# Optimization experiments

Hardware: AMD Instinct MI355X
Metric: run time of the kernel (lower is better)

Reference implementation:

```python
import jax, jax.numpy as jnp
import numpy as np

IDIM = 1024
ODIM = 1024
NHEADS = 16
B, S = 4, 1024


def setup_inputs() -> dict:
    key = jax.random.key(0)
    k1, k2, k3, k4, k5, k6 = jax.random.split(key, 6)
    m_feats = jax.random.normal(k1, (B, S, IDIM), dtype=jnp.float32)
    mask = jax.random.randint(k2, (B, S), 0, 2, dtype=jnp.int32)
    # torch Linear weights stored pre-transposed: y = x @ W + b
    W_c = jax.random.normal(k3, (IDIM, 2 * ODIM), dtype=jnp.float32) * 0.02
    b_c = jnp.zeros((2 * ODIM,), dtype=jnp.float32)
    W_v = jax.random.normal(k4, (IDIM, ODIM), dtype=jnp.float32) * 0.02
    b_v = jnp.zeros((ODIM,), dtype=jnp.float32)
    return {"m_feats": m_feats, "mask": mask, "W_c": W_c, "b_c": b_c, "W_v": W_v, "b_v": b_v}


def reference(m_feats, mask, W_c, b_c, W_v, b_v):
    # dp = 0.0 -> dropout is identity (eval-mode equivalence)
    Bn, Sn, _ = m_feats.shape
    odim = W_v.shape[1]
    dh = odim // NHEADS
    m_k = m_feats @ W_v + b_v            # v_lin  -> keys   [B,S,odim]
    m_trans = m_feats @ W_c + b_c        # c_lin  -> [B,S,2*odim]
    m_q = m_trans[..., :odim]            # queries
    m_v = m_trans[..., odim:]            # values
    mk = m_k.reshape(Bn, Sn, NHEADS, dh)
    mq = m_q.reshape(Bn, Sn, NHEADS, dh)
    mv = m_v.reshape(Bn, Sn, NHEADS, dh)
    # original: scores = K @ Q^T / sqrt(dh); softmax over the Q (last) axis
    scores = jnp.einsum('bihd,bjhd->bhij', mk, mq) / jnp.sqrt(jnp.float32(dh))
    maskf = mask.astype(jnp.float32)
    scores = jnp.where(maskf[:, None, None, :] == 0.0, jnp.float32(-1e9), scores)
    w = jax.nn.softmax(scores, axis=-1)               # [B,H,S,S]
    r = jnp.einsum('bhij,bjhd->bihd', w, mv).reshape(Bn, Sn, odim)
    updated_m = m_feats + r
    return updated_m, w
```

## Files before the change

kernel.cpp:

```cpp
#include <hip/hip_runtime.h>
#include <cstddef>

typedef short short8 __attribute__((ext_vector_type(8)));
typedef float f32x4 __attribute__((ext_vector_type(4)));

#define SS 1024
#define NH 16
#define DH 64
#define NB 4

static __device__ __forceinline__ unsigned short f2bf(float f) {
    union { float f; unsigned int i; } x; x.f = f;
    unsigned int r = x.i + 0x7FFFu + ((x.i >> 16) & 1u);
    return (unsigned short)(r >> 16);
}
static __device__ __forceinline__ float bf2f(unsigned short u) {
    union { unsigned int i; float f; } x; x.i = ((unsigned int)u) << 16;
    return x.f;
}

static __device__ __forceinline__ void g2l16(const void* g, void* l) {
    __builtin_amdgcn_global_load_lds(
        (const __attribute__((address_space(1))) unsigned int*)g,
        (__attribute__((address_space(3))) unsigned int*)l, 16, 0, 0);
}

__global__ __launch_bounds__(256) void prep(const float* __restrict__ mf,
                                            unsigned short* __restrict__ mfb,
                                            const float* __restrict__ Wv,
                                            const float* __restrict__ Wc,
                                            unsigned short* __restrict__ WT) {
    __shared__ float tile[32][33];
    int bx = blockIdx.x;
    int t = threadIdx.x;
    if (bx < 2048) {
        size_t i = ((size_t)bx * 256 + t) * 8;
        float4 v0 = *(const float4*)(mf + i);
        float4 v1 = *(const float4*)(mf + i + 4);
        short8 o;
        o[0] = (short)f2bf(v0.x); o[1] = (short)f2bf(v0.y);
        o[2] = (short)f2bf(v0.z); o[3] = (short)f2bf(v0.w);
        o[4] = (short)f2bf(v1.x); o[5] = (short)f2bf(v1.y);
        o[6] = (short)f2bf(v1.z); o[7] = (short)f2bf(v1.w);
        *(short8*)(mfb + i) = o;
        return;
    }
    bx -= 2048;
    int n0 = (bx % 96) * 32, k0 = (bx / 96) * 32;
    int kr = t >> 3, nc = (t & 7) * 4;
    const float* src; int ld; int nn = n0 + nc;
    if (n0 < 1024) { src = Wv; ld = 1024; } else { src = Wc; ld = 2048; nn -= 1024; }
    float4 v = *(const float4*)(src + (size_t)(k0 + kr) * ld + nn);
    tile[kr][nc + 0] = v.x; tile[kr][nc + 1] = v.y;
    tile[kr][nc + 2] = v.z; tile[kr][nc + 3] = v.w;
    __syncthreads();
    int nr = t >> 3, kc = (t & 7) * 4;
    short4 o;
    o.x = (short)f2bf(tile[kc + 0][nr]); o.y = (short)f2bf(tile[kc + 1][nr]);
    o.z = (short)f2bf(tile[kc + 2][nr]); o.w = (short)f2bf(tile[kc + 3][nr]);
    *(short4*)(WT + (size_t)(n0 + nr) * 1024 + k0 + kc) = o;
}

__global__ __launch_bounds__(256) void gemm_kqv(const unsigned short* __restrict__ A,
                                                const unsigned short* __restrict__ BT,
                                                const float* __restrict__ bv,
                                                const float* __restrict__ bc,
                                                unsigned short* __restrict__ kq,
                                                unsigned short* __restrict__ mvT) {
    __shared__ __align__(16) unsigned short As[2][128 * 32];
    __shared__ __align__(16) unsigned short Bs[2][128 * 32];
    int lin = blockIdx.y * 24 + blockIdx.x;
    int xcd = lin & 7, idx = lin >> 3;
    int cx = xcd & 1, cy = xcd >> 1;
    int xi = idx % 12, yi = idx / 12;
    int n0 = (cx * 12 + xi) * 128;
    int m0 = (cy * 8 + yi) * 128;

    int tid = threadIdx.x, lane = tid & 63, wv = tid >> 6;
    int wm = wv >> 1, wn = wv & 1;
    int lq = lane & 15, quad = lane >> 4;

    f32x4 zero = {0.f, 0.f, 0.f, 0.f};
    f32x4 acc[4][4];
#pragma unroll
    for (int i = 0; i < 4; ++i)
#pragma unroll
        for (int j = 0; j < 4; ++j) acc[i][j] = zero;

    int r0 = tid >> 2, s0 = tid & 3;
    int c0 = s0 ^ ((r0 >> 1) & 3);
    int r1 = (tid + 256) >> 2, s1 = tid & 3;
    int c1 = s1 ^ ((r1 >> 1) & 3);

    const unsigned short* Abase0 = A + (size_t)(m0 + r0) * 1024 + c0 * 8;
    const unsigned short* Abase1 = A + (size_t)(m0 + r1) * 1024 + c1 * 8;
    const unsigned short* Bbase0 = BT + (size_t)(n0 + r0) * 1024 + c0 * 8;
    const unsigned short* Bbase1 = BT + (size_t)(n0 + r1) * 1024 + c1 * 8;

    g2l16(Abase0, As[0] + tid * 8);
    g2l16(Abase1, As[0] + (tid + 256) * 8);
    g2l16(Bbase0, Bs[0] + tid * 8);
    g2l16(Bbase1, Bs[0] + (tid + 256) * 8);
    __syncthreads();

#pragma unroll 2
    for (int t32 = 0; t32 < 32; ++t32) {
        int cur = t32 & 1;
        if (t32 < 31) {
            int nkt = (t32 + 1) * 32;
            g2l16(Abase0 + nkt, As[cur ^ 1] + tid * 8);
            g2l16(Abase1 + nkt, As[cur ^ 1] + (tid + 256) * 8);
            g2l16(Bbase0 + nkt, Bs[cur ^ 1] + tid * 8);
            g2l16(Bbase1 + nkt, Bs[cur ^ 1] + (tid + 256) * 8);
        }

        short8 af[4], bfr[4];
#pragma unroll
        for (int i = 0; i < 4; ++i) {
            int Ra = wm * 64 + i * 16 + lq;
            af[i] = *(const short8*)(As[cur] + Ra * 32 + (quad ^ ((Ra >> 1) & 3)) * 8);
            int Rb = wn * 64 + i * 16 + lq;
            bfr[i] = *(const short8*)(Bs[cur] + Rb * 32 + (quad ^ ((Rb >> 1) & 3)) * 8);
        }
#pragma unroll
        for (int mi = 0; mi < 4; ++mi)
#pragma unroll
            for (int ni = 0; ni < 4; ++ni)
                acc[mi][ni] = __builtin_amdgcn_mfma_f32_16x16x32_bf16(af[mi], bfr[ni], acc[mi][ni], 0, 0, 0);

        __syncthreads();
    }

#pragma unroll
    for (int mi = 0; mi < 4; ++mi) {
#pragma unroll
        for (int ni = 0; ni < 4; ++ni) {
            int colg = n0 + wn * 64 + ni * 16 + lq;
            float bias = (colg < 1024) ? bv[colg] : bc[colg - 1024];
            if (colg < 2048) {
#pragma unroll
                for (int r = 0; r < 4; ++r) {
                    int rowg = m0 + wm * 64 + mi * 16 + quad * 4 + r;
                    kq[(size_t)rowg * 2048 + colg] = f2bf(acc[mi][ni][r] + bias);
                }
            } else {
                int c = colg - 2048;
                int hh = c >> 6, dd = c & 63;
#pragma unroll
                for (int r = 0; r < 4; ++r) {
                    int rowg = m0 + wm * 64 + mi * 16 + quad * 4 + r;
                    int bb = rowg >> 10, jj = rowg & 1023;
                    mvT[((size_t)(bb * NH + hh) * DH + dd) * 1024 + jj] =
                        f2bf(acc[mi][ni][r] + bias);
                }
            }
        }
    }
}

__global__ __launch_bounds__(256, 2) void attn_kernel(const unsigned short* __restrict__ kq,
                                                      const unsigned short* __restrict__ mvT,
                                                      const int* __restrict__ mask,
                                                      const float* __restrict__ m_feats,
                                                      float* __restrict__ out0,
                                                      float* __restrict__ out1) {
    __shared__ __align__(16) unsigned short mk_s[32 * 72];
    __shared__ __align__(16) unsigned short s_exp[32 * 1032];
    __shared__ float wsum[4][32];
    __shared__ float inv_s[32];

    int tid = threadIdx.x;
    int lane = tid & 63, wv = tid >> 6;
    int lq = lane & 15, quad = lane >> 4;

    int blk = ((int)blockIdx.x & 7) * 256 + ((int)blockIdx.x >> 3);
    int it = blk & 31;
    int bh = blk >> 5;
    int h = bh & (NH - 1), b = bh >> 4;
    int i0 = it * 32;

    const float SC = 0.18033688011112042f;
    const unsigned short* mqb = kq + (size_t)b * SS * 2048 + 1024 + h * 64 + quad * 8;
    const int* maskb = mask + (size_t)b * SS;

    short8 qb[2][4][2];
    int qm[2][4];
    float sums[2][4] = {{0.f, 0.f, 0.f, 0.f}, {0.f, 0.f, 0.f, 0.f}};

#define QLOAD(p, s)                                                          \
    {                                                                        \
        int jb_ = (s) * 256 + wv * 64;                                       \
        _Pragma("unroll") for (int js = 0; js < 4; ++js) {                   \
            int jg_ = jb_ + js * 16 + lq;                                    \
            size_t ro_ = (size_t)jg_ * 2048;                                 \
            qb[p][js][0] = *(const short8*)(mqb + ro_);                      \
            qb[p][js][1] = *(const short8*)(mqb + ro_ + 32);                 \
            qm[p][js] = maskb[jg_];                                          \
        }                                                                    \
    }

#define QCOMP(p, s)                                                          \
    {                                                                        \
        int jb_ = (s) * 256 + wv * 64;                                       \
        _Pragma("unroll") for (int js = 0; js < 4; ++js) {                   \
            int jc_ = jb_ + js * 16 + lq;                                    \
            _Pragma("unroll") for (int ti = 0; ti < 2; ++ti) {               \
                f32x4 acc = {0.f, 0.f, 0.f, 0.f};                            \
                acc = __builtin_amdgcn_mfma_f32_16x16x32_bf16(a[ti][0], qb[p][js][0], acc, 0, 0, 0); \
                acc = __builtin_amdgcn_mfma_f32_16x16x32_bf16(a[ti][1], qb[p][js][1], acc, 0, 0, 0); \
                _Pragma("unroll") for (int r = 0; r < 4; ++r) {              \
                    float e = qm[p][js] ? __builtin_amdgcn_exp2f(acc[r] * SC) : 0.f; \
                    sums[ti][r] += e;                                        \
                    s_exp[(ti * 16 + quad * 4 + r) * 1032 + jc_] = f2bf(e);  \
                }                                                            \
            }                                                                \
        }                                                                    \
    }

    QLOAD(0, 0);

    float mf8[2][4];
#pragma unroll
    for (int ti = 0; ti < 2; ++ti)
#pragma unroll
        for (int r = 0; r < 4; ++r) {
            size_t o = (size_t)(b * SS + i0 + ti * 16 + quad * 4 + r) * 1024 + h * 64 + wv * 16 + lq;
            mf8[ti][r] = m_feats[o];
        }

    {
        int row = tid >> 3, ch = tid & 7;
        int4 v = *(const int4*)(kq + (size_t)(b * SS + i0 + row) * 2048 + h * 64 + ch * 8);
        *(int4*)(mk_s + row * 72 + ch * 8) = v;
    }
    QLOAD(1, 1);
    __syncthreads();

    short8 a[2][2];
#pragma unroll
    for (int ti = 0; ti < 2; ++ti) {
        a[ti][0] = *(const short8*)(mk_s + (ti * 16 + lq) * 72 + 0 * 32 + quad * 8);
        a[ti][1] = *(const short8*)(mk_s + (ti * 16 + lq) * 72 + 1 * 32 + quad * 8);
    }

    QCOMP(0, 0); QLOAD(0, 2);
    QCOMP(1, 1); QLOAD(1, 3);
    QCOMP(0, 2);
    QCOMP(1, 3);
#undef QLOAD
#undef QCOMP

    f32x4 racc[2] = {{0.f, 0.f, 0.f, 0.f}, {0.f, 0.f, 0.f, 0.f}};
    const unsigned short* mvb = mvT + ((size_t)bh * DH + wv * 16 + lq) * 1024 + quad * 8;
    size_t wbase = ((size_t)bh * SS + i0) * SS;
    short8 vbuf[4][4];

#define VLOAD(p, ko)                                                         \
    {                                                                        \
        _Pragma("unroll") for (int k2 = 0; k2 < 4; ++k2)                     \
            vbuf[p][k2] = *(const short8*)(mvb + ((ko) * 4 + k2) * 32);      \
    }

#define VCOMP(p, ko)                                                         \
    {                                                                        \
        _Pragma("unroll") for (int k2 = 0; k2 < 4; ++k2) {                   \
            _Pragma("unroll") for (int ti = 0; ti < 2; ++ti) {               \
                short8 ae = *(const short8*)(s_exp + (ti * 16 + lq) * 1032 + ((ko) * 4 + k2) * 32 + quad * 8); \
                racc[ti] = __builtin_amdgcn_mfma_f32_16x16x32_bf16(ae, vbuf[p][k2], racc[ti], 0, 0, 0); \
            }                                                                \
        }                                                                    \
    }

#define WOUT(r)                                                              \
    {                                                                        \
        float iv = inv_s[r];                                                 \
        short4 ev = *(const short4*)(s_exp + (r) * 1032 + tid * 4);          \
        f32x4 wo;                                                            \
        wo[0] = bf2f((unsigned short)ev.x) * iv;                             \
        wo[1] = bf2f((unsigned short)ev.y) * iv;                             \
        wo[2] = bf2f((unsigned short)ev.z) * iv;                             \
        wo[3] = bf2f((unsigned short)ev.w) * iv;                             \
        __builtin_nontemporal_store(wo, (f32x4*)(out1 + wbase + (size_t)(r) * SS + tid * 4)); \
    }

    VLOAD(0, 0); VLOAD(1, 1);

#pragma unroll
    for (int ti = 0; ti < 2; ++ti)
#pragma unroll
        for (int r = 0; r < 4; ++r) {
            float s = sums[ti][r];
            s += __shfl_xor(s, 1); s += __shfl_xor(s, 2);
            s += __shfl_xor(s, 4); s += __shfl_xor(s, 8);
            if (lq == 0) wsum[wv][ti * 16 + quad * 4 + r] = s;
        }
    __syncthreads();
    if (tid < 32) {
        float s = wsum[0][tid] + wsum[1][tid] + wsum[2][tid] + wsum[3][tid];
        inv_s[tid] = 1.0f / s;
    }
    VLOAD(2, 2); VLOAD(3, 3);
    __syncthreads();

    VCOMP(0, 0); VLOAD(0, 4); WOUT(0);  WOUT(1);  WOUT(2);  WOUT(3);
    VCOMP(1, 1); VLOAD(1, 5); WOUT(4);  WOUT(5);  WOUT(6);  WOUT(7);
    VCOMP(2, 2); VLOAD(2, 6); WOUT(8);  WOUT(9);  WOUT(10); WOUT(11);
    VCOMP(3, 3); VLOAD(3, 7); WOUT(12); WOUT(13); WOUT(14); WOUT(15);
    VCOMP(0, 4); WOUT(16); WOUT(17); WOUT(18); WOUT(19);
    VCOMP(1, 5); WOUT(20); WOUT(21); WOUT(22); WOUT(23);
    VCOMP(2, 6); WOUT(24); WOUT(25); WOUT(26); WOUT(27);
    VCOMP(3, 7); WOUT(28); WOUT(29); WOUT(30); WOUT(31);
#undef VLOAD
#undef VCOMP
#undef WOUT

#pragma unroll
    for (int ti = 0; ti < 2; ++ti)
#pragma unroll
        for (int r = 0; r < 4; ++r) {
            int row = ti * 16 + quad * 4 + r;
            size_t o = (size_t)(b * SS + i0 + row) * 1024 + h * 64 + wv * 16 + lq;
            __builtin_nontemporal_store(mf8[ti][r] + racc[ti][r] * inv_s[row], out0 + o);
        }
}

extern "C" void kernel_launch(void* const* d_in, const int* in_sizes, int n_in,
                              void* d_out, int out_size, void* d_ws, size_t ws_size,
                              hipStream_t stream) {
    const float* m_feats = (const float*)d_in[0];
    const int*   mask    = (const int*)d_in[1];
    const float* W_c     = (const float*)d_in[2];
    const float* b_c     = (const float*)d_in[3];
    const float* W_v     = (const float*)d_in[4];
    const float* b_v     = (const float*)d_in[5];

    float* out0 = (float*)d_out;
    float* out1 = out0 + (size_t)NB * SS * 1024;

    unsigned short* mf_bf = (unsigned short*)d_ws;
    unsigned short* WT    = mf_bf + (size_t)4096 * 1024;
    unsigned short* kq    = WT + (size_t)3072 * 1024;
    unsigned short* mvT   = kq + (size_t)4096 * 2048;

    prep<<<dim3(5120), dim3(256), 0, stream>>>(m_feats, mf_bf, W_v, W_c, WT);
    gemm_kqv<<<dim3(24, 32), dim3(256), 0, stream>>>(mf_bf, WT, b_v, b_c, kq, mvT);
    attn_kernel<<<dim3(2048), dim3(256), 0, stream>>>(kq, mvT, mask, m_feats, out0, out1);
}
```

Measured before the change: 375.4 us.

## Double attention row tile to 64 rows with 512-thread blocks

Each attention block now covers 64 query rows using 8 waves instead of 32 rows with 4 waves. Every loaded Q tile is reused across twice as many score rows, which halves the global reads of the Q and V operands per output. The cost is a larger LDS footprint (about 132KB of s_exp), one block per CU, more registers per thread, and a shallower load pipeline in the score phase.

```diff
diff --git a/kernel.cpp b/kernel.cpp
--- a/kernel.cpp
+++ b/kernel.cpp
@@ -158,26 +158,26 @@
     }
 }
 
-__global__ __launch_bounds__(256, 2) void attn_kernel(const unsigned short* __restrict__ kq,
+__global__ __launch_bounds__(512, 1) void attn_kernel(const unsigned short* __restrict__ kq,
                                                       const unsigned short* __restrict__ mvT,
                                                       const int* __restrict__ mask,
                                                       const float* __restrict__ m_feats,
                                                       float* __restrict__ out0,
                                                       float* __restrict__ out1) {
-    __shared__ __align__(16) unsigned short mk_s[32 * 72];
-    __shared__ __align__(16) unsigned short s_exp[32 * 1032];
-    __shared__ float wsum[4][32];
-    __shared__ float inv_s[32];
+    __shared__ __align__(16) unsigned short mk_s[64 * 72];
+    __shared__ __align__(16) unsigned short s_exp[64 * 1032];
+    __shared__ float wsum[8][64];
+    __shared__ float inv_s[64];
 
     int tid = threadIdx.x;
     int lane = tid & 63, wv = tid >> 6;
     int lq = lane & 15, quad = lane >> 4;
 
-    int blk = ((int)blockIdx.x & 7) * 256 + ((int)blockIdx.x >> 3);
-    int it = blk & 31;
-    int bh = blk >> 5;
+    int blk = ((int)blockIdx.x & 7) * 128 + ((int)blockIdx.x >> 3);
+    int it = blk & 15;
+    int bh = blk >> 4;
     int h = bh & (NH - 1), b = bh >> 4;
-    int i0 = it * 32;
+    int i0 = it * 64;
 
     const float SC = 0.18033688011112042f;
     const unsigned short* mqb = kq + (size_t)b * SS * 2048 + 1024 + h * 64 + quad * 8;
@@ -185,11 +185,11 @@
 
     short8 qb[2][4][2];
     int qm[2][4];
-    float sums[2][4] = {{0.f, 0.f, 0.f, 0.f}, {0.f, 0.f, 0.f, 0.f}};
+    float sums[4][4] = {{0.f,0.f,0.f,0.f},{0.f,0.f,0.f,0.f},{0.f,0.f,0.f,0.f},{0.f,0.f,0.f,0.f}};
 
 #define QLOAD(p, s)                                                          \
     {                                                                        \
-        int jb_ = (s) * 256 + wv * 64;                                       \
+        int jb_ = (s) * 512 + wv * 64;                                       \
         _Pragma("unroll") for (int js = 0; js < 4; ++js) {                   \
             int jg_ = jb_ + js * 16 + lq;                                    \
             size_t ro_ = (size_t)jg_ * 2048;                                 \
@@ -201,10 +201,10 @@
 
 #define QCOMP(p, s)                                                          \
     {                                                                        \
-        int jb_ = (s) * 256 + wv * 64;                                       \
+        int jb_ = (s) * 512 + wv * 64;                                       \
         _Pragma("unroll") for (int js = 0; js < 4; ++js) {                   \
             int jc_ = jb_ + js * 16 + lq;                                    \
-            _Pragma("unroll") for (int ti = 0; ti < 2; ++ti) {               \
+            _Pragma("unroll") for (int ti = 0; ti < 4; ++ti) {               \
                 f32x4 acc = {0.f, 0.f, 0.f, 0.f};                            \
                 acc = __builtin_amdgcn_mfma_f32_16x16x32_bf16(a[ti][0], qb[p][js][0], acc, 0, 0, 0); \
                 acc = __builtin_amdgcn_mfma_f32_16x16x32_bf16(a[ti][1], qb[p][js][1], acc, 0, 0, 0); \
@@ -219,13 +219,15 @@
 
     QLOAD(0, 0);
 
+    int wq = wv & 3, tp = wv >> 2;
     float mf8[2][4];
 #pragma unroll
-    for (int ti = 0; ti < 2; ++ti)
+    for (int tt = 0; tt < 2; ++tt)
 #pragma unroll
         for (int r = 0; r < 4; ++r) {
-            size_t o = (size_t)(b * SS + i0 + ti * 16 + quad * 4 + r) * 1024 + h * 64 + wv * 16 + lq;
-            mf8[ti][r] = m_feats[o];
+            size_t o = (size_t)(b * SS + i0 + (tp * 2 + tt) * 16 + quad * 4 + r) * 1024
+                       + h * 64 + wq * 16 + lq;
+            mf8[tt][r] = m_feats[o];
         }
 
     {
@@ -236,22 +238,20 @@
     QLOAD(1, 1);
     __syncthreads();
 
-    short8 a[2][2];
-#pragma unroll
-    for (int ti = 0; ti < 2; ++ti) {
+    short8 a[4][2];
+#pragma unroll
+    for (int ti = 0; ti < 4; ++ti) {
         a[ti][0] = *(const short8*)(mk_s + (ti * 16 + lq) * 72 + 0 * 32 + quad * 8);
         a[ti][1] = *(const short8*)(mk_s + (ti * 16 + lq) * 72 + 1 * 32 + quad * 8);
     }
 
-    QCOMP(0, 0); QLOAD(0, 2);
-    QCOMP(1, 1); QLOAD(1, 3);
-    QCOMP(0, 2);
-    QCOMP(1, 3);
+    QCOMP(0, 0);
+    QCOMP(1, 1);
 #undef QLOAD
 #undef QCOMP
 
     f32x4 racc[2] = {{0.f, 0.f, 0.f, 0.f}, {0.f, 0.f, 0.f, 0.f}};
-    const unsigned short* mvb = mvT + ((size_t)bh * DH + wv * 16 + lq) * 1024 + quad * 8;
+    const unsigned short* mvb = mvT + ((size_t)bh * DH + wq * 16 + lq) * 1024 + quad * 8;
     size_t wbase = ((size_t)bh * SS + i0) * SS;
     short8 vbuf[4][4];
 
@@ -264,29 +264,30 @@
 #define VCOMP(p, ko)                                                         \
     {                                                                        \
         _Pragma("unroll") for (int k2 = 0; k2 < 4; ++k2) {                   \
-            _Pragma("unroll") for (int ti = 0; ti < 2; ++ti) {               \
-                short8 ae = *(const short8*)(s_exp + (ti * 16 + lq) * 1032 + ((ko) * 4 + k2) * 32 + quad * 8); \
-                racc[ti] = __builtin_amdgcn_mfma_f32_16x16x32_bf16(ae, vbuf[p][k2], racc[ti], 0, 0, 0); \
+            _Pragma("unroll") for (int tt = 0; tt < 2; ++tt) {               \
+                short8 ae = *(const short8*)(s_exp + ((tp * 2 + tt) * 16 + lq) * 1032 + ((ko) * 4 + k2) * 32 + quad * 8); \
+                racc[tt] = __builtin_amdgcn_mfma_f32_16x16x32_bf16(ae, vbuf[p][k2], racc[tt], 0, 0, 0); \
             }                                                                \
         }                                                                    \
     }
 
-#define WOUT(r)                                                              \
-    {                                                                        \
-        float iv = inv_s[r];                                                 \
-        short4 ev = *(const short4*)(s_exp + (r) * 1032 + tid * 4);          \
+#define WOUT(pr)                                                             \
+    {                                                                        \
+        int row_ = (pr) * 2 + (tid >> 8);                                    \
+        float iv = inv_s[row_];                                              \
+        short4 ev = *(const short4*)(s_exp + row_ * 1032 + (tid & 255) * 4); \
         f32x4 wo;                                                            \
         wo[0] = bf2f((unsigned short)ev.x) * iv;                             \
         wo[1] = bf2f((unsigned short)ev.y) * iv;                             \
         wo[2] = bf2f((unsigned short)ev.z) * iv;                             \
         wo[3] = bf2f((unsigned short)ev.w) * iv;                             \
-        __builtin_nontemporal_store(wo, (f32x4*)(out1 + wbase + (size_t)(r) * SS + tid * 4)); \
+        __builtin_nontemporal_store(wo, (f32x4*)(out1 + wbase + (size_t)row_ * SS + (tid & 255) * 4)); \
     }
 
     VLOAD(0, 0); VLOAD(1, 1);
 
 #pragma unroll
-    for (int ti = 0; ti < 2; ++ti)
+    for (int ti = 0; ti < 4; ++ti)
 #pragma unroll
         for (int r = 0; r < 4; ++r) {
             float s = sums[ti][r];
@@ -295,8 +296,9 @@
             if (lq == 0) wsum[wv][ti * 16 + quad * 4 + r] = s;
         }
     __syncthreads();
-    if (tid < 32) {
-        float s = wsum[0][tid] + wsum[1][tid] + wsum[2][tid] + wsum[3][tid];
+    if (tid < 64) {
+        float s = wsum[0][tid] + wsum[1][tid] + wsum[2][tid] + wsum[3][tid]
+                + wsum[4][tid] + wsum[5][tid] + wsum[6][tid] + wsum[7][tid];
         inv_s[tid] = 1.0f / s;
     }
     VLOAD(2, 2); VLOAD(3, 3);
@@ -315,12 +317,12 @@
 #undef WOUT
 
 #pragma unroll
-    for (int ti = 0; ti < 2; ++ti)
+    for (int tt = 0; tt < 2; ++tt)
 #pragma unroll
         for (int r = 0; r < 4; ++r) {
-            int row = ti * 16 + quad * 4 + r;
-            size_t o = (size_t)(b * SS + i0 + row) * 1024 + h * 64 + wv * 16 + lq;
-            __builtin_nontemporal_store(mf8[ti][r] + racc[ti][r] * inv_s[row], out0 + o);
+            int row = (tp * 2 + tt) * 16 + quad * 4 + r;
+            size_t o = (size_t)(b * SS + i0 + row) * 1024 + h * 64 + wq * 16 + lq;
+            __builtin_nontemporal_store(mf8[tt][r] + racc[tt][r] * inv_s[row], out0 + o);
         }
 }
 
@@ -344,5 +346,5 @@
 
     prep<<<dim3(5120), dim3(256), 0, stream>>>(m_feats, mf_bf, W_v, W_c, WT);
     gemm_kqv<<<dim3(24, 32), dim3(256), 0, stream>>>(mf_bf, WT, b_v, b_c, kq, mvT);
-    attn_kernel<<<dim3(2048), dim3(256), 0, stream>>>(kq, mvT, mask, m_feats, out0, out1);
-}
+    attn_kernel<<<dim3(1024), dim3(512), 0, stream>>>(kq, mvT, mask, m_feats, out0, out1);
+}
```

Result: slower. 399.4 us (+6.4%).

## Split score computation into two row halves to overlap weight stores with compute

Applied to the files above, without the earlier changes.

The QK^T/exp phase now runs per 16-row half. After the first half, its row sums are reduced and its normalized softmax rows are streamed to the attention-weight output while the second half's scores are computed. This starts the large weight-matrix writes earlier instead of holding them all until the PV phase. In exchange, Q tiles are loaded twice, there is an extra reduction with barriers, and register pressure rises.

```diff
diff --git a/kernel.cpp b/kernel.cpp
--- a/kernel.cpp
+++ b/kernel.cpp
@@ -166,7 +166,7 @@
                                                       float* __restrict__ out1) {
     __shared__ __align__(16) unsigned short mk_s[32 * 72];
     __shared__ __align__(16) unsigned short s_exp[32 * 1032];
-    __shared__ float wsum[4][32];
+    __shared__ float wsum[4][16];
     __shared__ float inv_s[32];
 
     int tid = threadIdx.x;
@@ -199,20 +199,18 @@
         }                                                                    \
     }
 
-#define QCOMP(p, s)                                                          \
+#define QCOMPH(p, s, TI)                                                     \
     {                                                                        \
         int jb_ = (s) * 256 + wv * 64;                                       \
         _Pragma("unroll") for (int js = 0; js < 4; ++js) {                   \
             int jc_ = jb_ + js * 16 + lq;                                    \
-            _Pragma("unroll") for (int ti = 0; ti < 2; ++ti) {               \
-                f32x4 acc = {0.f, 0.f, 0.f, 0.f};                            \
-                acc = __builtin_amdgcn_mfma_f32_16x16x32_bf16(a[ti][0], qb[p][js][0], acc, 0, 0, 0); \
-                acc = __builtin_amdgcn_mfma_f32_16x16x32_bf16(a[ti][1], qb[p][js][1], acc, 0, 0, 0); \
-                _Pragma("unroll") for (int r = 0; r < 4; ++r) {              \
-                    float e = qm[p][js] ? __builtin_amdgcn_exp2f(acc[r] * SC) : 0.f; \
-                    sums[ti][r] += e;                                        \
-                    s_exp[(ti * 16 + quad * 4 + r) * 1032 + jc_] = f2bf(e);  \
-                }                                                            \
+            f32x4 acc = {0.f, 0.f, 0.f, 0.f};                                \
+            acc = __builtin_amdgcn_mfma_f32_16x16x32_bf16(a[TI][0], qb[p][js][0], acc, 0, 0, 0); \
+            acc = __builtin_amdgcn_mfma_f32_16x16x32_bf16(a[TI][1], qb[p][js][1], acc, 0, 0, 0); \
+            _Pragma("unroll") for (int r = 0; r < 4; ++r) {                  \
+                float e = qm[p][js] ? __builtin_amdgcn_exp2f(acc[r] * SC) : 0.f; \
+                sums[TI][r] += e;                                            \
+                s_exp[((TI) * 16 + quad * 4 + r) * 1032 + jc_] = f2bf(e);    \
             }                                                                \
         }                                                                    \
     }
@@ -243,33 +241,24 @@
         a[ti][1] = *(const short8*)(mk_s + (ti * 16 + lq) * 72 + 1 * 32 + quad * 8);
     }
 
-    QCOMP(0, 0); QLOAD(0, 2);
-    QCOMP(1, 1); QLOAD(1, 3);
-    QCOMP(0, 2);
-    QCOMP(1, 3);
-#undef QLOAD
-#undef QCOMP
-
-    f32x4 racc[2] = {{0.f, 0.f, 0.f, 0.f}, {0.f, 0.f, 0.f, 0.f}};
-    const unsigned short* mvb = mvT + ((size_t)bh * DH + wv * 16 + lq) * 1024 + quad * 8;
-    size_t wbase = ((size_t)bh * SS + i0) * SS;
-    short8 vbuf[4][4];
-
-#define VLOAD(p, ko)                                                         \
-    {                                                                        \
-        _Pragma("unroll") for (int k2 = 0; k2 < 4; ++k2)                     \
-            vbuf[p][k2] = *(const short8*)(mvb + ((ko) * 4 + k2) * 32);      \
-    }
-
-#define VCOMP(p, ko)                                                         \
-    {                                                                        \
-        _Pragma("unroll") for (int k2 = 0; k2 < 4; ++k2) {                   \
-            _Pragma("unroll") for (int ti = 0; ti < 2; ++ti) {               \
-                short8 ae = *(const short8*)(s_exp + (ti * 16 + lq) * 1032 + ((ko) * 4 + k2) * 32 + quad * 8); \
-                racc[ti] = __builtin_amdgcn_mfma_f32_16x16x32_bf16(ae, vbuf[p][k2], racc[ti], 0, 0, 0); \
-            }                                                                \
-        }                                                                    \
-    }
+    QCOMPH(0, 0, 0); QLOAD(0, 2);
+    QCOMPH(1, 1, 0); QLOAD(1, 3);
+    QCOMPH(0, 2, 0); QLOAD(0, 0);
+    QCOMPH(1, 3, 0); QLOAD(1, 1);
+
+#pragma unroll
+    for (int r = 0; r < 4; ++r) {
+        float s = sums[0][r];
+        s += __shfl_xor(s, 1); s += __shfl_xor(s, 2);
+        s += __shfl_xor(s, 4); s += __shfl_xor(s, 8);
+        if (lq == 0) wsum[wv][quad * 4 + r] = s;
+    }
+    __syncthreads();
+    if (tid < 16) {
+        float s = wsum[0][tid] + wsum[1][tid] + wsum[2][tid] + wsum[3][tid];
+        inv_s[tid] = 1.0f / s;
+    }
+    __syncthreads();
 
 #define WOUT(r)                                                              \
     {                                                                        \
@@ -283,33 +272,60 @@
         __builtin_nontemporal_store(wo, (f32x4*)(out1 + wbase + (size_t)(r) * SS + tid * 4)); \
     }
 
+    size_t wbase = ((size_t)bh * SS + i0) * SS;
+
+    QCOMPH(0, 0, 1); QLOAD(0, 2); WOUT(0);  WOUT(1);  WOUT(2);  WOUT(3);
+    QCOMPH(1, 1, 1); QLOAD(1, 3); WOUT(4);  WOUT(5);  WOUT(6);  WOUT(7);
+    QCOMPH(0, 2, 1); WOUT(8);  WOUT(9);  WOUT(10); WOUT(11);
+    QCOMPH(1, 3, 1); WOUT(12); WOUT(13); WOUT(14); WOUT(15);
+#undef QLOAD
+#undef QCOMPH
+
+    f32x4 racc[2] = {{0.f, 0.f, 0.f, 0.f}, {0.f, 0.f, 0.f, 0.f}};
+    const unsigned short* mvb = mvT + ((size_t)bh * DH + wv * 16 + lq) * 1024 + quad * 8;
+    short8 vbuf[4][4];
+
+#define VLOAD(p, ko)                                                         \
+    {                                                                        \
+        _Pragma("unroll") for (int k2 = 0; k2 < 4; ++k2)                     \
+            vbuf[p][k2] = *(const short8*)(mvb + ((ko) * 4 + k2) * 32);      \
+    }
+
+#define VCOMP(p, ko)                                                         \
+    {                                                                        \
+        _Pragma("unroll") for (int k2 = 0; k2 < 4; ++k2) {                   \
+            _Pragma("unroll") for (int ti = 0; ti < 2; ++ti) {               \
+                short8 ae = *(const short8*)(s_exp + (ti * 16 + lq) * 1032 + ((ko) * 4 + k2) * 32 + quad * 8); \
+                racc[ti] = __builtin_amdgcn_mfma_f32_16x16x32_bf16(ae, vbuf[p][k2], racc[ti], 0, 0, 0); \
+            }                                                                \
+        }                                                                    \
+    }
+
     VLOAD(0, 0); VLOAD(1, 1);
 
 #pragma unroll
-    for (int ti = 0; ti < 2; ++ti)
-#pragma unroll
-        for (int r = 0; r < 4; ++r) {
-            float s = sums[ti][r];
-            s += __shfl_xor(s, 1); s += __shfl_xor(s, 2);
-            s += __shfl_xor(s, 4); s += __shfl_xor(s, 8);
-            if (lq == 0) wsum[wv][ti * 16 + quad * 4 + r] = s;
-        }
-    __syncthreads();
-    if (tid < 32) {
+    for (int r = 0; r < 4; ++r) {
+        float s = sums[1][r];
+        s += __shfl_xor(s, 1); s += __shfl_xor(s, 2);
+        s += __shfl_xor(s, 4); s += __shfl_xor(s, 8);
+        if (lq == 0) wsum[wv][quad * 4 + r] = s;
+    }
+    __syncthreads();
+    if (tid < 16) {
         float s = wsum[0][tid] + wsum[1][tid] + wsum[2][tid] + wsum[3][tid];
-        inv_s[tid] = 1.0f / s;
+        inv_s[16 + tid] = 1.0f / s;
     }
     VLOAD(2, 2); VLOAD(3, 3);
     __syncthreads();
 
-    VCOMP(0, 0); VLOAD(0, 4); WOUT(0);  WOUT(1);  WOUT(2);  WOUT(3);
-    VCOMP(1, 1); VLOAD(1, 5); WOUT(4);  WOUT(5);  WOUT(6);  WOUT(7);
-    VCOMP(2, 2); VLOAD(2, 6); WOUT(8);  WOUT(9);  WOUT(10); WOUT(11);
-    VCOMP(3, 3); VLOAD(3, 7); WOUT(12); WOUT(13); WOUT(14); WOUT(15);
-    VCOMP(0, 4); WOUT(16); WOUT(17); WOUT(18); WOUT(19);
-    VCOMP(1, 5); WOUT(20); WOUT(21); WOUT(22); WOUT(23);
-    VCOMP(2, 6); WOUT(24); WOUT(25); WOUT(26); WOUT(27);
-    VCOMP(3, 7); WOUT(28); WOUT(29); WOUT(30); WOUT(31);
+    VCOMP(0, 0); VLOAD(0, 4); WOUT(16); WOUT(17);
+    VCOMP(1, 1); VLOAD(1, 5); WOUT(18); WOUT(19);
+    VCOMP(2, 2); VLOAD(2, 6); WOUT(20); WOUT(21);
+    VCOMP(3, 3); VLOAD(3, 7); WOUT(22); WOUT(23);
+    VCOMP(0, 4); WOUT(24); WOUT(25);
+    VCOMP(1, 5); WOUT(26); WOUT(27);
+    VCOMP(2, 6); WOUT(28); WOUT(29);
+    VCOMP(3, 7); WOUT(30); WOUT(31);
 #undef VLOAD
 #undef VCOMP
 #undef WOUT
```

After: 397.0 us. 5.7% more time.
